# Kernel optimization log

Hardware: AMD Instinct MI355X
Metric: run time of the kernel (lower is better)

Reference implementation:

```python
import jax, jax.numpy as jnp
import numpy as np

RECALL_THRESHOLD = 0.3
LAMBDA_PAUC = 0.5
NUM_CLASSES = 128
LABEL_SMOOTHING = 0.1
N_SAMPLES = 131072


def setup_inputs() -> dict:
    key = jax.random.key(0)
    k1, k2 = jax.random.split(key)
    predictions = jax.random.normal(k1, (N_SAMPLES, NUM_CLASSES), dtype=jnp.float32)
    targets = jax.random.randint(k2, (N_SAMPLES,), 0, NUM_CLASSES)
    return {"predictions": predictions, "targets": targets}


def _macro_pauc(probs, targets):
    """Vectorized (over classes) partial AUC at max_fpr = 1 - recall_threshold.

    Equivalent to the per-class torch loop: descending argsort of scores,
    cumsum TP/FP, clip the ROC curve at max_fpr with linear interpolation of
    the crossing segment, trapezoidal integration, macro-average over classes
    that have at least one positive.
    """
    N, K = probs.shape
    order = jnp.argsort(-probs, axis=0)                      # [N, K] descending per class
    t_sorted = (targets[order] == jnp.arange(K)[None, :]).astype(probs.dtype)  # [N, K]
    tps = jnp.cumsum(t_sorted, axis=0)                        # [N, K]
    fps = jnp.cumsum(1.0 - t_sorted, axis=0)                  # [N, K]
    tpr = tps / jnp.maximum(tps[-1], 1.0)
    fpr = fps / jnp.maximum(fps[-1], 1.0)

    max_fpr = 1.0 - RECALL_THRESHOLD
    # Clip fpr at max_fpr; segments fully beyond the cut get delta == 0 so
    # their tpr value is irrelevant. The crossing segment's right endpoint is
    # replaced by the linearly interpolated tpr at max_fpr (matches torch's
    # slope-based interpolation with the same 1e-8 guard).
    fpr_c = jnp.minimum(fpr, max_fpr)
    slope = (tpr[1:] - tpr[:-1]) / (fpr[1:] - fpr[:-1] + 1e-8)
    tpr_interp = tpr[:-1] + slope * (max_fpr - fpr[:-1])
    tpr_next = jnp.where(fpr[1:] <= max_fpr, tpr[1:], tpr_interp)
    delta = fpr_c[1:] - fpr_c[:-1]                            # [N-1, K]
    pauc_c = jnp.sum(delta * 0.5 * (tpr_next + tpr[:-1]), axis=0)  # [K]

    valid = (tps[-1] > 0).astype(probs.dtype)                 # macro: skip empty classes
    return jnp.sum(pauc_c * valid) / jnp.maximum(jnp.sum(valid), 1.0)


def reference(predictions, targets):
    logp = jax.nn.log_softmax(predictions, axis=1)
    probs = jnp.exp(logp)
    # CrossEntropyLoss with label smoothing (mean reduction, no class weights):
    # loss_i = (1-eps) * nll_i + eps * mean_c(-log p_ic)
    nll = -jnp.take_along_axis(logp, targets[:, None], axis=1)[:, 0]
    smooth = -jnp.mean(logp, axis=1)
    ce_loss = jnp.mean((1.0 - LABEL_SMOOTHING) * nll + LABEL_SMOOTHING * smooth)

    # torch.tensor(pauc) in the original detaches pAUC from the graph.
    pauc = jax.lax.stop_gradient(_macro_pauc(probs, targets))
    pauc_loss = 1.0 - pauc ** 2
    return (1.0 - LAMBDA_PAUC) * ce_loss + LAMBDA_PAUC * pauc_loss
```

## Files before the change

kernel.cpp:

```cpp
#include <hip/hip_runtime.h>
#include <math.h>

#define N_SAMPLES 131072
#define NUM_CLASSES 128
#define NB 256
#define MAX_FPR 0.7f
#define NBLK 512
#define ROWS_PER_BLK 256
#define HWORDS (NB / 2)
#define HPITCH 129
#define PART_WORDS (NUM_CLASSES * HWORDS)

__device__ __forceinline__ int bin_of(float x, float off ) {
    int b = (int)__fmaf_rn(x, 16.0f, off);
    return min(max(b, 0), NB - 1);
}

__global__ __launch_bounds__(512, 4) void fused_kernel(
    const float* __restrict__ pred, const int* __restrict__ tgt,
    unsigned int* __restrict__ hPos,
    unsigned int* __restrict__ part,
    float* __restrict__ ce_accum)
{
    __shared__ unsigned int h32[NUM_CLASSES * HPITCH];
    __shared__ float wsum[8];

    const int tid  = threadIdx.x;
    const int w    = tid >> 6;
    const int lane = tid & 63;
    const int j    = lane & 15;
    const int rs   = lane >> 4;

    for (int i = tid; i < NUM_CLASSES * HPITCH; i += 512) h32[i] = 0u;
    __syncthreads();

    const int rowBase = blockIdx.x * ROWS_PER_BLK + w * 4 + rs;

    float acc_lse = 0.0f, acc_xt = 0.0f, acc_sx = 0.0f;

    const float* rp = pred + (size_t)rowBase * 128;
    float4 a0 = *(const float4*)(rp + j * 4);
    float4 a1 = *(const float4*)(rp + 64 + j * 4);
    int    tc = tgt[rowBase];

    #pragma unroll
    for (int p = 0; p < 8; p++) {
        float4 b0, b1; int tn = 0;
        if (p < 7) {
            const float* rn = pred + (size_t)(rowBase + (p + 1) * 32) * 128;
            b0 = *(const float4*)(rn + j * 4);
            b1 = *(const float4*)(rn + 64 + j * 4);
            tn = tgt[rowBase + (p + 1) * 32];
        }

        float e = __expf(a0.x) + __expf(a0.y) + __expf(a0.z) + __expf(a0.w)
                + __expf(a1.x) + __expf(a1.y) + __expf(a1.z) + __expf(a1.w);
        #pragma unroll
        for (int o = 1; o < 16; o <<= 1) e += __shfl_xor(e, o);
        const float lse = __logf(e);
        const float off = (14.0f - lse) * 16.0f;

        const float xv[8] = {a0.x, a0.y, a0.z, a0.w, a1.x, a1.y, a1.z, a1.w};
        #pragma unroll
        for (int q = 0; q < 8; q++) {
            const int c = (q < 4) ? (j * 4 + q) : (64 + j * 4 + (q - 4));
            const int b = bin_of(xv[q], off);
            atomicAdd(&h32[c * HPITCH + (b >> 1)], (b & 1) ? 65536u : 1u);
        }

        acc_sx += (xv[0] + xv[1] + xv[2] + xv[3])
                + (xv[4] + xv[5] + xv[6] + xv[7]);
        if (j == 0) acc_lse += lse;

        {
            const int t = tc;
            float xt; bool hit = false;
            if ((t >> 2) == j)                        { xt = xv[t & 3];       hit = true; }
            else if (t >= 64 && ((t - 64) >> 2) == j) { xt = xv[4 + (t & 3)]; hit = true; }
            if (hit) {
                acc_xt += xt;
                atomicAdd(&hPos[(t << 8) | bin_of(xt, off)], 1u);
            }
        }

        a0 = b0; a1 = b1; tc = tn;
    }

    float ce = acc_lse - 0.9f * acc_xt - (0.1f / 128.0f) * acc_sx;
    #pragma unroll
    for (int o = 32; o; o >>= 1) ce += __shfl_xor(ce, o);
    if (lane == 0) wsum[w] = ce;
    __syncthreads();

    if (tid == 0) {
        float s = 0.0f;
        #pragma unroll
        for (int i = 0; i < 8; i++) s += wsum[i];
        atomicAdd(ce_accum, s);
    }

    unsigned int* out = part + (size_t)blockIdx.x * PART_WORDS;
    for (int i = tid; i < PART_WORDS; i += 512)
        out[i] = h32[(i >> 7) * HPITCH + (i & 127)];
}

__global__ __launch_bounds__(256) void pauc_reduce(
    const unsigned int* __restrict__ part,
    const unsigned int* __restrict__ hPos,
    float* __restrict__ acc,
    float* __restrict__ out)
{
    __shared__ __align__(16) unsigned int sA[NB];

    const int k    = blockIdx.x;
    const int t    = threadIdx.x;
    const int w    = t & 127;
    const int half = t >> 7;

    unsigned int lo = 0u, hi = 0u;
    const unsigned int* p0 = part + (size_t)(half * (NBLK / 2)) * PART_WORDS
                                  + k * HWORDS + w;
    #pragma unroll 8
    for (int b = 0; b < NBLK / 2; b++) {
        const unsigned int q = p0[(size_t)b * PART_WORDS];
        lo += q & 0xffffu; hi += q >> 16;
    }
    if (half == 0) { sA[2 * w] = lo; sA[2 * w + 1] = hi; }
    __syncthreads();
    if (half == 1) { sA[2 * w] += lo; sA[2 * w + 1] += hi; }
    __syncthreads();

    if (t < 64) {
        const int lane = t;
        const uint4 q  = ((const uint4*)sA)[63 - lane];
        const unsigned int a[4] = {q.w, q.z, q.y, q.x};
        const uint4 pq = ((const uint4*)(hPos + (k << 8)))[63 - lane];
        const unsigned int p[4] = {pq.w, pq.z, pq.y, pq.x};

        const unsigned int la = a[0] + a[1] + a[2] + a[3];
        const unsigned int lp = p[0] + p[1] + p[2] + p[3];

        unsigned int ia = la, ip = lp;
        #pragma unroll
        for (int o = 1; o < 64; o <<= 1) {
            const unsigned int ta = __shfl_up(ia, o);
            const unsigned int tp = __shfl_up(ip, o);
            if (lane >= o) { ia += ta; ip += tp; }
        }
        const unsigned int P = __shfl(ip, 63);
        const unsigned int T = __shfl(ia, 63);
        const float Pm = fmaxf((float)P, 1.0f);
        const float Fm = fmaxf((float)(T - P), 1.0f);

        int cumA = (int)(ia - la), cumP = (int)(ip - lp);
        float contrib = 0.0f;
        #pragma unroll
        for (int i = 0; i < 4; i++) {
            const int f = (int)a[i] - (int)p[i];
            if (f > 0) {
                const float fpr0 = (float)(cumA - cumP) / Fm;
                if (fpr0 < MAX_FPR) {
                    const float tpr0 = (float)cumP / Pm;
                    const float tpr1 = (float)(cumP + (int)p[i]) / Pm;
                    const float fpr1 = (float)(cumA - cumP + f) / Fm;
                    if (fpr1 <= MAX_FPR) {
                        contrib += (fpr1 - fpr0) * 0.5f * (tpr0 + tpr1);
                    } else {
                        const float tfrac = (MAX_FPR - fpr0) / (fpr1 - fpr0);
                        const float tprc  = tpr0 + tfrac * (tpr1 - tpr0);
                        contrib += (MAX_FPR - fpr0) * 0.5f * (tpr0 + tprc);
                    }
                }
            }
            cumA += (int)a[i]; cumP += (int)p[i];
        }

        #pragma unroll
        for (int o = 32; o; o >>= 1) contrib += __shfl_xor(contrib, o);

        if (lane == 0) {
            if (P > 0u) {
                atomicAdd(&acc[1], contrib);
                atomicAdd(&acc[2], 1.0f);
            }
            __threadfence();
            const unsigned int done = atomicAdd((unsigned int*)(acc + 3), 1u);
            if (done == NUM_CLASSES - 1) {
                const float ces = atomicAdd(&acc[0], 0.0f);
                const float ps  = atomicAdd(&acc[1], 0.0f);
                const float vs  = atomicAdd(&acc[2], 0.0f);
                const float ce   = ces * (1.0f / (float)N_SAMPLES);
                const float pauc = ps / fmaxf(vs, 1.0f);
                out[0] = 0.5f * ce + 0.5f * (1.0f - pauc * pauc);
            }
        }
    }
}

extern "C" void kernel_launch(void* const* d_in, const int* in_sizes, int n_in,
                              void* d_out, int out_size, void* d_ws, size_t ws_size,
                              hipStream_t stream)
{
    const float* pred = (const float*)d_in[0];
    const int*   tgt  = (const int*)d_in[1];

    char* ws = (char*)d_ws;
    unsigned int* hPos = (unsigned int*)ws;
    float*        acc  = (float*)(ws + 131072);
    unsigned int* part = (unsigned int*)(ws + 262144);

    hipMemsetAsync(hPos, 0, 131072 + 16, stream);

    fused_kernel<<<NBLK, 512, 0, stream>>>(pred, tgt, hPos, part, acc);
    pauc_reduce<<<NUM_CLASSES, 256, 0, stream>>>(part, hPos, acc, (float*)d_out);
}
```

Before: 116.5 us.

## Fuse histogram reduction into main kernel with global atomics and grid barrier

Merges the two-kernel pipeline into one launch. Each block now adds its shared histogram directly into a global 64-bit packed histogram with atomics instead of writing per-block partials. The first 128 blocks then spin-wait on a completion counter and compute the per-class pAUC. Blocks grow to 1024 threads covering 512 rows, with a two-deep prefetch. This removes the second launch and the large partial-buffer traffic, but it relies on all 256 blocks being co-resident for the spin barrier and adds global atomic contention.

```diff
diff --git a/kernel.cpp b/kernel.cpp
--- a/kernel.cpp
+++ b/kernel.cpp
@@ -5,25 +5,27 @@
 #define NUM_CLASSES 128
 #define NB 256
 #define MAX_FPR 0.7f
-#define NBLK 512
-#define ROWS_PER_BLK 256
-#define HWORDS (NB / 2)
+#define NBLK 256
+#define ROWS_PER_BLK 512
 #define HPITCH 129
-#define PART_WORDS (NUM_CLASSES * HWORDS)
+
+typedef unsigned long long u64;
+typedef unsigned int u32;
 
 __device__ __forceinline__ int bin_of(float x, float off ) {
     int b = (int)__fmaf_rn(x, 16.0f, off);
     return min(max(b, 0), NB - 1);
 }
 
-__global__ __launch_bounds__(512, 4) void fused_kernel(
+__global__ __launch_bounds__(1024, 4) void fused_all(
     const float* __restrict__ pred, const int* __restrict__ tgt,
-    unsigned int* __restrict__ hPos,
-    unsigned int* __restrict__ part,
-    float* __restrict__ ce_accum)
+    u64* __restrict__ hAll,
+    u32* __restrict__ hPos,
+    float* __restrict__ acc,
+    float* __restrict__ out)
 {
-    __shared__ unsigned int h32[NUM_CLASSES * HPITCH];
-    __shared__ float wsum[8];
+    __shared__ u32 h32[NUM_CLASSES * HPITCH];
+    __shared__ float wsum[16];
 
     const int tid  = threadIdx.x;
     const int w    = tid >> 6;
@@ -31,26 +33,29 @@
     const int j    = lane & 15;
     const int rs   = lane >> 4;
 
-    for (int i = tid; i < NUM_CLASSES * HPITCH; i += 512) h32[i] = 0u;
+    for (int i = tid; i < NUM_CLASSES * HPITCH; i += 1024) h32[i] = 0u;
     __syncthreads();
 
     const int rowBase = blockIdx.x * ROWS_PER_BLK + w * 4 + rs;
-
     float acc_lse = 0.0f, acc_xt = 0.0f, acc_sx = 0.0f;
 
-    const float* rp = pred + (size_t)rowBase * 128;
-    float4 a0 = *(const float4*)(rp + j * 4);
-    float4 a1 = *(const float4*)(rp + 64 + j * 4);
-    int    tc = tgt[rowBase];
+    const float* r0p = pred + (size_t)rowBase * 128;
+    float4 a0 = *(const float4*)(r0p + j * 4);
+    float4 a1 = *(const float4*)(r0p + 64 + j * 4);
+    int    ta = tgt[rowBase];
+    const float* r1p = r0p + (size_t)64 * 128;
+    float4 c0 = *(const float4*)(r1p + j * 4);
+    float4 c1 = *(const float4*)(r1p + 64 + j * 4);
+    int    tb = tgt[rowBase + 64];
 
     #pragma unroll
     for (int p = 0; p < 8; p++) {
-        float4 b0, b1; int tn = 0;
-        if (p < 7) {
-            const float* rn = pred + (size_t)(rowBase + (p + 1) * 32) * 128;
-            b0 = *(const float4*)(rn + j * 4);
-            b1 = *(const float4*)(rn + 64 + j * 4);
-            tn = tgt[rowBase + (p + 1) * 32];
+        float4 n0, n1; int tn = 0;
+        if (p < 6) {
+            const float* rn = pred + (size_t)(rowBase + (p + 2) * 64) * 128;
+            n0 = *(const float4*)(rn + j * 4);
+            n1 = *(const float4*)(rn + 64 + j * 4);
+            tn = tgt[rowBase + (p + 2) * 64];
         }
 
         float e = __expf(a0.x) + __expf(a0.y) + __expf(a0.z) + __expf(a0.w)
@@ -68,12 +73,12 @@
             atomicAdd(&h32[c * HPITCH + (b >> 1)], (b & 1) ? 65536u : 1u);
         }
 
-        acc_sx += (xv[0] + xv[1] + xv[2] + xv[3])
-                + (xv[4] + xv[5] + xv[6] + xv[7]);
-        if (j == 0) acc_lse += lse;
+        acc_sx  += (xv[0] + xv[1] + xv[2] + xv[3])
+                 + (xv[4] + xv[5] + xv[6] + xv[7]);
+        acc_lse += lse * 0.0625f;
 
         {
-            const int t = tc;
+            const int t = ta;
             float xt; bool hit = false;
             if ((t >> 2) == j)                        { xt = xv[t & 3];       hit = true; }
             else if (t >= 64 && ((t - 64) >> 2) == j) { xt = xv[4 + (t & 3)]; hit = true; }
@@ -83,7 +88,8 @@
             }
         }
 
-        a0 = b0; a1 = b1; tc = tn;
+        a0 = c0; a1 = c1; ta = tb;
+        c0 = n0; c1 = n1; tb = tn;
     }
 
     float ce = acc_lse - 0.9f * acc_xt - (0.1f / 128.0f) * acc_sx;
@@ -91,64 +97,60 @@
     for (int o = 32; o; o >>= 1) ce += __shfl_xor(ce, o);
     if (lane == 0) wsum[w] = ce;
     __syncthreads();
-
     if (tid == 0) {
         float s = 0.0f;
         #pragma unroll
-        for (int i = 0; i < 8; i++) s += wsum[i];
-        atomicAdd(ce_accum, s);
-    }
-
-    unsigned int* out = part + (size_t)blockIdx.x * PART_WORDS;
-    for (int i = tid; i < PART_WORDS; i += 512)
-        out[i] = h32[(i >> 7) * HPITCH + (i & 127)];
-}
-
-__global__ __launch_bounds__(256) void pauc_reduce(
-    const unsigned int* __restrict__ part,
-    const unsigned int* __restrict__ hPos,
-    float* __restrict__ acc,
-    float* __restrict__ out)
-{
-    __shared__ __align__(16) unsigned int sA[NB];
-
-    const int k    = blockIdx.x;
-    const int t    = threadIdx.x;
-    const int w    = t & 127;
-    const int half = t >> 7;
-
-    unsigned int lo = 0u, hi = 0u;
-    const unsigned int* p0 = part + (size_t)(half * (NBLK / 2)) * PART_WORDS
-                                  + k * HWORDS + w;
-    #pragma unroll 8
-    for (int b = 0; b < NBLK / 2; b++) {
-        const unsigned int q = p0[(size_t)b * PART_WORDS];
-        lo += q & 0xffffu; hi += q >> 16;
-    }
-    if (half == 0) { sA[2 * w] = lo; sA[2 * w + 1] = hi; }
-    __syncthreads();
-    if (half == 1) { sA[2 * w] += lo; sA[2 * w + 1] += hi; }
-    __syncthreads();
-
-    if (t < 64) {
-        const int lane = t;
-        const uint4 q  = ((const uint4*)sA)[63 - lane];
-        const unsigned int a[4] = {q.w, q.z, q.y, q.x};
-        const uint4 pq = ((const uint4*)(hPos + (k << 8)))[63 - lane];
-        const unsigned int p[4] = {pq.w, pq.z, pq.y, pq.x};
-
-        const unsigned int la = a[0] + a[1] + a[2] + a[3];
-        const unsigned int lp = p[0] + p[1] + p[2] + p[3];
-
-        unsigned int ia = la, ip = lp;
+        for (int i = 0; i < 16; i++) s += wsum[i];
+        atomicAdd(&acc[0], s);
+    }
+
+    for (int i = tid; i < NUM_CLASSES * 128; i += 1024) {
+        const u32 v = h32[(i >> 7) * HPITCH + (i & 127)];
+        if (v) atomicAdd(&hAll[i], (u64)(v & 0xffffu) | ((u64)(v >> 16) << 32));
+    }
+
+    __syncthreads();
+    if (tid == 0) {
+        __threadfence();
+        atomicAdd((u32*)(acc + 3), 1u);
+    }
+    if (blockIdx.x >= NUM_CLASSES) return;
+
+    if (tid == 0) {
+        while (__hip_atomic_load((u32*)(acc + 3), __ATOMIC_ACQUIRE,
+                                 __HIP_MEMORY_SCOPE_AGENT) < NBLK)
+            __builtin_amdgcn_s_sleep(2);
+    }
+    __syncthreads();
+    __threadfence();
+
+    if (tid < 64) {
+        const int l = tid;
+        const int k = blockIdx.x;
+        const u64* hPos64 = (const u64*)hPos;
+        const u64 wA1 = __hip_atomic_load(&hAll[k * 128 + 127 - 2 * l],
+                                          __ATOMIC_RELAXED, __HIP_MEMORY_SCOPE_AGENT);
+        const u64 wA0 = __hip_atomic_load(&hAll[k * 128 + 126 - 2 * l],
+                                          __ATOMIC_RELAXED, __HIP_MEMORY_SCOPE_AGENT);
+        const u64 wP1 = __hip_atomic_load(&hPos64[k * 128 + 127 - 2 * l],
+                                          __ATOMIC_RELAXED, __HIP_MEMORY_SCOPE_AGENT);
+        const u64 wP0 = __hip_atomic_load(&hPos64[k * 128 + 126 - 2 * l],
+                                          __ATOMIC_RELAXED, __HIP_MEMORY_SCOPE_AGENT);
+        const u32 a[4] = {(u32)(wA1 >> 32), (u32)wA1, (u32)(wA0 >> 32), (u32)wA0};
+        const u32 p[4] = {(u32)(wP1 >> 32), (u32)wP1, (u32)(wP0 >> 32), (u32)wP0};
+
+        const u32 la = a[0] + a[1] + a[2] + a[3];
+        const u32 lp = p[0] + p[1] + p[2] + p[3];
+
+        u32 ia = la, ip = lp;
         #pragma unroll
         for (int o = 1; o < 64; o <<= 1) {
-            const unsigned int ta = __shfl_up(ia, o);
-            const unsigned int tp = __shfl_up(ip, o);
-            if (lane >= o) { ia += ta; ip += tp; }
-        }
-        const unsigned int P = __shfl(ip, 63);
-        const unsigned int T = __shfl(ia, 63);
+            const u32 tA = __shfl_up(ia, o);
+            const u32 tP = __shfl_up(ip, o);
+            if (l >= o) { ia += tA; ip += tP; }
+        }
+        const u32 P = __shfl(ip, 63);
+        const u32 T = __shfl(ia, 63);
         const float Pm = fmaxf((float)P, 1.0f);
         const float Fm = fmaxf((float)(T - P), 1.0f);
 
@@ -178,20 +180,20 @@
         #pragma unroll
         for (int o = 32; o; o >>= 1) contrib += __shfl_xor(contrib, o);
 
-        if (lane == 0) {
+        if (l == 0) {
             if (P > 0u) {
                 atomicAdd(&acc[1], contrib);
                 atomicAdd(&acc[2], 1.0f);
             }
             __threadfence();
-            const unsigned int done = atomicAdd((unsigned int*)(acc + 3), 1u);
+            const u32 done = atomicAdd((u32*)(acc + 4), 1u);
             if (done == NUM_CLASSES - 1) {
                 const float ces = atomicAdd(&acc[0], 0.0f);
                 const float ps  = atomicAdd(&acc[1], 0.0f);
                 const float vs  = atomicAdd(&acc[2], 0.0f);
-                const float ce   = ces * (1.0f / (float)N_SAMPLES);
+                const float cem  = ces * (1.0f / (float)N_SAMPLES);
                 const float pauc = ps / fmaxf(vs, 1.0f);
-                out[0] = 0.5f * ce + 0.5f * (1.0f - pauc * pauc);
+                out[0] = 0.5f * cem + 0.5f * (1.0f - pauc * pauc);
             }
         }
     }
@@ -205,12 +207,10 @@
     const int*   tgt  = (const int*)d_in[1];
 
     char* ws = (char*)d_ws;
-    unsigned int* hPos = (unsigned int*)ws;
-    float*        acc  = (float*)(ws + 131072);
-    unsigned int* part = (unsigned int*)(ws + 262144);
-
-    hipMemsetAsync(hPos, 0, 131072 + 16, stream);
-
-    fused_kernel<<<NBLK, 512, 0, stream>>>(pred, tgt, hPos, part, acc);
-    pauc_reduce<<<NUM_CLASSES, 256, 0, stream>>>(part, hPos, acc, (float*)d_out);
+    u64*   hAll = (u64*)ws;
+    u32*   hPos = (u32*)(ws + 131072);
+    float* acc  = (float*)(ws + 262144);
+
+    hipMemsetAsync(ws, 0, 262144 + 32, stream);
+    fused_all<<<NBLK, 1024, 0, stream>>>(pred, tgt, hAll, hPos, acc, (float*)d_out);
 }
```

After: 154.3 us. +32.4%, slower.
